# Kernel optimization log

Measured on AMD Instinct MI355X. Metric: run time of the kernel, lower is better.

The kernel has to match this reference:

```python
import jax, jax.numpy as jnp
import numpy as np

VOCAB = 128000
SEED = 42
BATCH = 256
SEQ = 128
BIAS_FACTOR = 2.0
TOP_P = 0.9


def setup_inputs() -> dict:
    key = jax.random.key(0)
    k1, k2 = jax.random.split(key)
    input_ids = jax.random.randint(k1, (BATCH, SEQ), 0, VOCAB, dtype=jnp.int64 if jax.config.jax_enable_x64 else jnp.int32)
    scores = jax.random.normal(k2, (BATCH, VOCAB), dtype=jnp.float32) * 4.0
    # green list generated exactly as in the torch module: numpy rng, 0/1 per vocab entry
    green = jnp.asarray(np.random.default_rng(SEED).integers(0, 2, VOCAB), dtype=jnp.float32)
    return {"input_ids": input_ids, "scores": scores, "green": green}


def reference(input_ids, scores, green):
    B, V = scores.shape
    # bias green tokens, softmax over vocab
    logits = scores + BIAS_FACTOR * green[None, :]          # [B, V]
    probs = jax.nn.softmax(logits, axis=-1)                 # [B, V]
    # descending sort (torch.sort(descending=True))
    sorted_idx = jnp.argsort(-probs, axis=-1)               # [B, V]
    sorted_probs = jnp.take_along_axis(probs, sorted_idx, axis=-1)
    cum = jnp.cumsum(sorted_probs, axis=-1)                 # [B, V]
    # torch.searchsorted(cum, top_p, right=False): first i with cum[i] >= top_p
    cutoff = jnp.sum(cum < TOP_P, axis=-1, keepdims=True)   # [B, 1]
    # keep positions 0..cutoff inclusive (original zeroes cutoff+1:)
    keep = jnp.arange(V)[None, :] <= cutoff                 # [B, V]
    kept = jnp.where(keep, sorted_probs, 0.0)
    kept = kept / jnp.sum(kept, axis=-1, keepdims=True)
    kept = jnp.where(jnp.isfinite(kept), kept, 0.0)
    # multinomial(1) over truncated renormalized probs
    samp = jax.random.categorical(jax.random.key(1), jnp.log(kept), axis=-1)  # [B]
    next_tok = jnp.take_along_axis(sorted_idx, samp[:, None], axis=-1)[:, 0]  # [B]
    # scores[b,:] = 1e-5; scores[b, next_token] = 1e5
    out = jnp.full((B, V), 1e-5, dtype=scores.dtype)
    out = out.at[jnp.arange(B), next_tok].set(1e5)
    return out
```

## Files before the change

### kernel.cpp

```cpp
#include <hip/hip_runtime.h>
#include <cstdint>
#include <cstddef>

#define BATCH 256
#define VOCAB 128000
#define V4 (VOCAB/4)
#define NBINS 4096
#define CAP 4096
#define WSEG 256
#define NSEG 32
#define SPILLCAP 6144
#define GATE_SPILL 8.0f
#define SPILL_BIN 3088u
#define GATE_HIST 1.0f
#define M44 0xFFFFFFFFFFFull
#define FIX 16777216.0f
#define FIXINV 5.9604644775390625e-8f

__device__ __forceinline__ uint32_t rotl32(uint32_t v, int r){ return (v<<r)|(v>>(32-r)); }

__device__ __forceinline__ void threefry2x32_01(uint32_t& x0, uint32_t& x1){
  const uint32_t ks0=0u, ks1=1u, ks2=0x1BD11BDAu ^ 0u ^ 1u;
  x0+=ks0; x1+=ks1;
#define TF_R(r) { x0+=x1; x1=rotl32(x1,(r)); x1^=x0; }
  TF_R(13) TF_R(15) TF_R(26) TF_R(6)
  x0+=ks1; x1+=ks2+1u;
  TF_R(17) TF_R(29) TF_R(16) TF_R(24)
  x0+=ks2; x1+=ks0+2u;
  TF_R(13) TF_R(15) TF_R(26) TF_R(6)
  x0+=ks0; x1+=ks1+3u;
  TF_R(17) TF_R(29) TF_R(16) TF_R(24)
  x0+=ks1; x1+=ks2+4u;
  TF_R(13) TF_R(15) TF_R(26) TF_R(6)
  x0+=ks2; x1+=ks0+5u;
#undef TF_R
}

__device__ __forceinline__ float gumbel_at(uint32_t z){
  uint32_t x0 = 0u, x1 = z;
  threefry2x32_01(x0, x1);
  uint32_t bits = x0 ^ x1;
  uint32_t fb = (bits >> 9) | 0x3F800000u;
  float f = __uint_as_float(fb) - 1.0f;
  const float tiny = 1.17549435e-38f;
  float uu = fmaxf(tiny, f + tiny);
  return -logf(-logf(uu));
}

__device__ __forceinline__ uint32_t fkey(uint32_t u){
  return (u >> 31) ? ~u : (u | 0x80000000u);
}
__device__ __forceinline__ float pdecode(unsigned long long k){
  return __uint_as_float(~(uint32_t)(k >> 32));
}

__global__ __launch_bounds__(256) void k_stream(
    const float* __restrict__ scores, const float* __restrict__ green,
    float* __restrict__ out, unsigned long long* __restrict__ spill,
    unsigned* __restrict__ counts, float* __restrict__ pmax,
    float* __restrict__ psum)
{
  const int blk = blockIdx.x;
  const int b = blk >> 3, q = blk & 7;
  const int tid = threadIdx.x, lane = tid & 63, wv = tid >> 6;
  const int base = q * 4000;
  const float4* row4 = (const float4*)(scores + (size_t)b * VOCAB);
  const float4* grn4 = (const float4*)green;
  float4* o4 = (float4*)(out + (size_t)b * VOCAB);
  const int sidx = (q << 2) | wv;
  unsigned long long* seg = spill + ((size_t)b * NSEG + sidx) * WSEG;
  const float4 fv = make_float4(1e-5f, 1e-5f, 1e-5f, 1e-5f);

  float lm = -INFINITY, ls16 = 0.f;
  unsigned wcnt = 0u;

#define SP1(LV, IDX) do { \
    float l_ = (LV); \
    lm = fmaxf(lm, l_); \
    ls16 += expf(l_ - 16.0f); \
    bool pr_ = (l_ >= GATE_SPILL); \
    unsigned long long mk_ = __ballot(pr_); \
    if (pr_){ \
      unsigned pos_ = wcnt + (unsigned)__popcll(mk_ & ((1ull << lane) - 1ull)); \
      if (pos_ < WSEG) \
        seg[pos_] = ((unsigned long long)__float_as_uint(l_) << 32) | (IDX); \
    } \
    wcnt += (unsigned)__popcll(mk_); \
  } while(0)

#define SP4(SV, GV, II) do { \
    SP1(fmaf(2.f, (GV).x, (SV).x), (unsigned)(4*(II)+0)); \
    SP1(fmaf(2.f, (GV).y, (SV).y), (unsigned)(4*(II)+1)); \
    SP1(fmaf(2.f, (GV).z, (SV).z), (unsigned)(4*(II)+2)); \
    SP1(fmaf(2.f, (GV).w, (SV).w), (unsigned)(4*(II)+3)); \
  } while(0)

  for (int g = 0; g < 3; ++g){
    const int i0 = base + tid + g*1024, i1 = i0+256, i2 = i0+512, i3 = i0+768;
    float4 sa = row4[i0], sb = row4[i1], sc = row4[i2], sd = row4[i3];
    float4 ga = grn4[i0], gb = grn4[i1], gc = grn4[i2], gd = grn4[i3];
    o4[i0] = fv; o4[i1] = fv; o4[i2] = fv; o4[i3] = fv;
    SP4(sa, ga, i0); SP4(sb, gb, i1); SP4(sc, gc, i2); SP4(sd, gd, i3);
  }
  {
    const int i0 = base + 3072 + tid, i1 = i0+256, i2 = i0+512;
    float4 sa = row4[i0], sb = row4[i1], sc = row4[i2];
    float4 ga = grn4[i0], gb = grn4[i1], gc = grn4[i2];
    o4[i0] = fv; o4[i1] = fv; o4[i2] = fv;
    SP4(sa, ga, i0); SP4(sb, gb, i1); SP4(sc, gc, i2);
  }
  if (tid < 160){
    const int i0 = base + 3840 + tid;
    float4 sa = row4[i0];
    float4 ga = grn4[i0];
    o4[i0] = fv;
    SP4(sa, ga, i0);
  }
#undef SP4
#undef SP1

  for (int off = 32; off > 0; off >>= 1){
    lm = fmaxf(lm, __shfl_down(lm, off, 64));
    ls16 += __shfl_down(ls16, off, 64);
  }
  if (lane == 0){
    const int gi = b * NSEG + sidx;
    pmax[gi] = lm; psum[gi] = ls16; counts[gi] = wcnt;
  }
}

__global__ __launch_bounds__(1024) void k_row(
    const float* __restrict__ scores, const float* __restrict__ green,
    float* __restrict__ out, const unsigned long long* __restrict__ spill,
    const unsigned* __restrict__ counts, const float* __restrict__ pmax,
    const float* __restrict__ psum)
{
  __shared__ unsigned long long sp64[SPILLCAP];
  __shared__ union {
    unsigned long long hist[NBINS];
    unsigned long long skeys[CAP];
  } u;
  __shared__ float red[1024];
  __shared__ unsigned long long wavewin[16];
  __shared__ unsigned segoff[NSEG + 1];
  __shared__ float m_sh, s16_sh;
  __shared__ unsigned n_sh, thr_sh, fb_sh;
  __shared__ int cut_sh;

  const int b = blockIdx.x, tid = threadIdx.x;
  const float* srow = scores + (size_t)b * VOCAB;
  float* orow = out + (size_t)b * VOCAB;

  for (int i = tid; i < NBINS; i += 1024) u.hist[i] = 0ull;
  if (tid == 0){
    unsigned tot = 0u, fb = 0u;
    float mm = -INFINITY, ss = 0.f;
    for (int s = 0; s < NSEG; ++s){
      unsigned c = counts[b*NSEG + s];
      segoff[s] = tot;
      if (c > WSEG) fb = 1u;
      tot += c;
      mm = fmaxf(mm, pmax[b*NSEG + s]);
      ss += psum[b*NSEG + s];
    }
    segoff[NSEG] = tot;
    if (tot > SPILLCAP) fb = 1u;
    m_sh = mm; s16_sh = ss; fb_sh = fb; n_sh = 0u;
  }
  __syncthreads();
  const float m = m_sh, S16 = s16_sh;
  const unsigned tot = segoff[NSEG];
  unsigned fb = fb_sh;

  if (!fb){
    for (int s = 0; s < NSEG; ++s){
      const unsigned c0 = segoff[s], cl = segoff[s+1] - c0;
      const unsigned long long* seg = spill + ((size_t)b*NSEG + s)*WSEG;
      for (unsigned j = tid; j < cl; j += 1024) sp64[c0 + j] = seg[j];
    }
    __syncthreads();
    for (unsigned j = tid; j < tot; j += 1024){
      uint32_t lb = (uint32_t)(sp64[j] >> 32);
      atomicAdd(&u.hist[fkey(lb) >> 20],
                (1ull<<44) | (unsigned long long)(expf(__uint_as_float(lb) - 16.0f) * FIX));
    }
    __syncthreads();
    if (tid == 0){
      float target = 0.903f * S16;
      int top = (int)(fkey(__float_as_uint(m)) >> 20);
      float acc = 0.f; unsigned c = 0; unsigned result = (unsigned)top;
      for (int bin = top; bin >= 0; --bin){
        unsigned long long h = u.hist[bin];
        unsigned cb = (unsigned)(h >> 44);
        if (c + cb > CAP) break;
        acc += (float)(h & M44) * FIXINV; c += cb; result = (unsigned)bin;
        if (acc >= target){
          if (bin > 0 && c + (unsigned)(u.hist[bin-1] >> 44) <= CAP)
            result = (unsigned)(bin-1);
          break;
        }
      }
      thr_sh = result;
      if (result < SPILL_BIN) fb_sh = 1u;
    }
    __syncthreads();
    fb = fb_sh;
  }

  if (fb){
    for (int i = tid; i < NBINS; i += 1024) u.hist[i] = 0ull;
    __syncthreads();
    const float4* row4 = (const float4*)srow;
    const float4* grn4 = (const float4*)green;
    for (int i = tid; i < V4; i += 1024){
      float4 s = row4[i], g = grn4[i];
      #pragma unroll
      for (int c = 0; c < 4; ++c){
        float l = fmaf(2.f, (&g.x)[c], (&s.x)[c]);
        if (l >= GATE_HIST)
          atomicAdd(&u.hist[fkey(__float_as_uint(l)) >> 20],
                    (1ull<<44) | (unsigned long long)(expf(l - 16.0f) * FIX));
      }
    }
    __syncthreads();
    if (tid == 0){
      float target = 0.903f * S16;
      int top = (int)(fkey(__float_as_uint(m)) >> 20);
      float acc = 0.f; unsigned c = 0; unsigned result = (unsigned)top;
      for (int bin = top; bin >= 0; --bin){
        unsigned long long h = u.hist[bin];
        unsigned cb = (unsigned)(h >> 44);
        if (c + cb > CAP) break;
        acc += (float)(h & M44) * FIXINV; c += cb; result = (unsigned)bin;
        if (acc >= target){
          if (bin > 0 && c + (unsigned)(u.hist[bin-1] >> 44) <= CAP)
            result = (unsigned)(bin-1);
          break;
        }
      }
      thr_sh = result;
    }
    __syncthreads();
    const unsigned thr = thr_sh;
    for (int i = tid; i < V4; i += 1024){
      float4 s = row4[i], g = grn4[i];
      #pragma unroll
      for (int c = 0; c < 4; ++c){
        float l = fmaf(2.f, (&g.x)[c], (&s.x)[c]);
        if ((fkey(__float_as_uint(l)) >> 20) >= thr){
          unsigned pos = atomicAdd(&n_sh, 1u);
          float p = expf(l - 16.0f) / S16;
          if (pos < CAP)
            u.skeys[pos] = ((unsigned long long)(~__float_as_uint(p)) << 32) | (unsigned)(4*i + c);
        }
      }
    }
  } else {
    const unsigned thr = thr_sh;
    for (unsigned j = tid; j < tot; j += 1024){
      unsigned long long k = sp64[j];
      uint32_t lb = (uint32_t)(k >> 32);
      if ((fkey(lb) >> 20) >= thr){
        unsigned pos = atomicAdd(&n_sh, 1u);
        float p = expf(__uint_as_float(lb) - 16.0f) / S16;
        if (pos < CAP)
          u.skeys[pos] = ((unsigned long long)(~__float_as_uint(p)) << 32) | (k & 0xFFFFFFFFull);
      }
    }
  }
  __syncthreads();
  unsigned n = n_sh; if (n > CAP) n = CAP;

  unsigned N2 = 2; while (N2 < n) N2 <<= 1;
  for (unsigned i = n + tid; i < N2; i += 1024) u.skeys[i] = 0xFFFFFFFFFFFFFFFFull;
  __syncthreads();
  for (unsigned k = 2; k <= N2; k <<= 1){
    for (unsigned j = k >> 1; j > 0; j >>= 1){
      for (unsigned i = tid; i < N2; i += 1024){
        unsigned ixj = i ^ j;
        if (ixj > i){
          unsigned long long a = u.skeys[i], c2 = u.skeys[ixj];
          bool up = ((i & k) == 0u);
          if ((a > c2) == up){ u.skeys[i] = c2; u.skeys[ixj] = a; }
        }
      }
      __syncthreads();
    }
  }

  unsigned C = (n + 1023) >> 10;
  {
    unsigned lo = tid * C; if (lo > n) lo = n;
    unsigned hi = lo + C;  if (hi > n) hi = n;
    float s = 0.f;
    for (unsigned j = lo; j < hi; ++j) s += pdecode(u.skeys[j]);
    red[tid] = s;
  }
  __syncthreads();
  if (tid == 0){
    float run = 0.f; int cut = (int)n - 1; int t = 0;
    for (; t < 1024; ++t){ float cs = red[t]; if (run + cs >= 0.9f) break; run += cs; }
    if (t < 1024){
      float c2 = run;
      for (unsigned j = (unsigned)t * C; j < n; ++j){
        c2 += pdecode(u.skeys[j]);
        if (c2 >= 0.9f){ cut = (int)j; break; }
      }
    }
    cut_sh = cut;
  }
  __syncthreads();
  const int cut = cut_sh;

  float best = -INFINITY; unsigned bj = 0x7FFFFFFFu;
  for (int j = tid; j <= cut; j += 1024){
    float p = pdecode(u.skeys[j]);
    float sc = logf(p) + gumbel_at((uint32_t)b * (uint32_t)VOCAB + (uint32_t)j);
    if (sc > best || (sc == best && (unsigned)j < bj)){ best = sc; bj = (unsigned)j; }
  }
  for (int off = 32; off > 0; off >>= 1){
    float osc = __shfl_down(best, off, 64);
    unsigned oj = __shfl_down(bj, off, 64);
    if (osc > best || (osc == best && oj < bj)){ best = osc; bj = oj; }
  }
  if ((tid & 63) == 0){
    uint32_t ub = __float_as_uint(best);
    uint32_t ou = (ub >> 31) ? ~ub : (ub | 0x80000000u);
    wavewin[tid >> 6] = ((unsigned long long)ou << 32) |
                        (unsigned long long)(0xFFFFFFFFu - bj);
  }
  __syncthreads();
  if (tid == 0){
    unsigned long long bb = 0ull;
    for (int w = 0; w < 16; ++w){ unsigned long long x = wavewin[w]; if (x > bb) bb = x; }
    unsigned jwin = 0xFFFFFFFFu - (unsigned)(bb & 0xFFFFFFFFull);
    orow[(size_t)(u.skeys[jwin] & 0xFFFFFFFFull)] = 1e5f;
  }
}

extern "C" void kernel_launch(void* const* d_in, const int* in_sizes, int n_in,
                              void* d_out, int out_size, void* d_ws, size_t ws_size,
                              hipStream_t stream) {
  const float* scores = (const float*)d_in[1];
  const float* green  = (const float*)d_in[2];
  float* out = (float*)d_out;

  unsigned long long* spill = (unsigned long long*)d_ws;
  unsigned* counts = (unsigned*)(spill + (size_t)BATCH * NSEG * WSEG);
  float* pmax = (float*)(counts + BATCH * NSEG);
  float* psum = pmax + BATCH * NSEG;
  (void)ws_size;

  hipLaunchKernelGGL(k_stream, dim3(BATCH*8), dim3(256),  0, stream,
                     scores, green, out, spill, counts, pmax, psum);
  hipLaunchKernelGGL(k_row,    dim3(BATCH),   dim3(1024), 0, stream,
                     scores, green, out, spill, counts, pmax, psum);
}
```

Measured before the change: 342.3 us.

## Software-pipeline stream loads, add occupancy hint, drop extra threshold bin

The streaming kernel now issues the next group's score and green loads before processing the current group, a register double-buffer meant to hide global memory latency. A launch-bounds occupancy hint of 4 blocks per CU is added. The threshold search in the row kernel no longer widens the candidate set by one extra histogram bin, which shrinks the candidate set to sort. That bin was a safety margin against approximate histogram sums, so dropping it risks correctness near the top-p cutoff, and the extra live registers could reduce occupancy.

```diff
diff --git a/kernel.cpp b/kernel.cpp
--- a/kernel.cpp
+++ b/kernel.cpp
@@ -54,7 +54,7 @@
   return __uint_as_float(~(uint32_t)(k >> 32));
 }
 
-__global__ __launch_bounds__(256) void k_stream(
+__global__ __launch_bounds__(256, 4) void k_stream(
     const float* __restrict__ scores, const float* __restrict__ green,
     float* __restrict__ out, unsigned long long* __restrict__ spill,
     unsigned* __restrict__ counts, float* __restrict__ pmax,
@@ -95,26 +95,40 @@
     SP1(fmaf(2.f, (GV).w, (SV).w), (unsigned)(4*(II)+3)); \
   } while(0)
 
+  float4 sa, sb, sc, sd, ga, gb, gc, gd;
+  {
+    const int i0 = base + tid;
+    sa = row4[i0]; sb = row4[i0+256]; sc = row4[i0+512]; sd = row4[i0+768];
+    ga = grn4[i0]; gb = grn4[i0+256]; gc = grn4[i0+512]; gd = grn4[i0+768];
+  }
+  #pragma unroll
   for (int g = 0; g < 3; ++g){
-    const int i0 = base + tid + g*1024, i1 = i0+256, i2 = i0+512, i3 = i0+768;
-    float4 sa = row4[i0], sb = row4[i1], sc = row4[i2], sd = row4[i3];
-    float4 ga = grn4[i0], gb = grn4[i1], gc = grn4[i2], gd = grn4[i3];
-    o4[i0] = fv; o4[i1] = fv; o4[i2] = fv; o4[i3] = fv;
-    SP4(sa, ga, i0); SP4(sb, gb, i1); SP4(sc, gc, i2); SP4(sd, gd, i3);
+    const int cur = base + tid + g*1024;
+    const int nxt = cur + 1024;
+    float4 ta, tb, tc, td, ua, ub, uc, ud;
+    if (g < 2){
+      ta = row4[nxt]; tb = row4[nxt+256]; tc = row4[nxt+512]; td = row4[nxt+768];
+      ua = grn4[nxt]; ub = grn4[nxt+256]; uc = grn4[nxt+512]; ud = grn4[nxt+768];
+    } else {
+      ta = row4[nxt]; tb = row4[nxt+256]; tc = row4[nxt+512];
+      ua = grn4[nxt]; ub = grn4[nxt+256]; uc = grn4[nxt+512];
+      td = tc; ud = uc;
+    }
+    o4[cur] = fv; o4[cur+256] = fv; o4[cur+512] = fv; o4[cur+768] = fv;
+    SP4(sa, ga, cur); SP4(sb, gb, cur+256); SP4(sc, gc, cur+512); SP4(sd, gd, cur+768);
+    sa = ta; sb = tb; sc = tc; sd = td; ga = ua; gb = ub; gc = uc; gd = ud;
   }
   {
-    const int i0 = base + 3072 + tid, i1 = i0+256, i2 = i0+512;
-    float4 sa = row4[i0], sb = row4[i1], sc = row4[i2];
-    float4 ga = grn4[i0], gb = grn4[i1], gc = grn4[i2];
-    o4[i0] = fv; o4[i1] = fv; o4[i2] = fv;
-    SP4(sa, ga, i0); SP4(sb, gb, i1); SP4(sc, gc, i2);
+    const int i0 = base + 3072 + tid;
+    o4[i0] = fv; o4[i0+256] = fv; o4[i0+512] = fv;
+    SP4(sa, ga, i0); SP4(sb, gb, i0+256); SP4(sc, gc, i0+512);
   }
   if (tid < 160){
     const int i0 = base + 3840 + tid;
-    float4 sa = row4[i0];
-    float4 ga = grn4[i0];
+    float4 s = row4[i0];
+    float4 g = grn4[i0];
     o4[i0] = fv;
-    SP4(sa, ga, i0);
+    SP4(s, g, i0);
   }
 #undef SP4
 #undef SP1
@@ -194,11 +208,7 @@
         unsigned cb = (unsigned)(h >> 44);
         if (c + cb > CAP) break;
         acc += (float)(h & M44) * FIXINV; c += cb; result = (unsigned)bin;
-        if (acc >= target){
-          if (bin > 0 && c + (unsigned)(u.hist[bin-1] >> 44) <= CAP)
-            result = (unsigned)(bin-1);
-          break;
-        }
+        if (acc >= target) break;
       }
       thr_sh = result;
       if (result < SPILL_BIN) fb_sh = 1u;
@@ -232,11 +242,7 @@
         unsigned cb = (unsigned)(h >> 44);
         if (c + cb > CAP) break;
         acc += (float)(h & M44) * FIXINV; c += cb; result = (unsigned)bin;
-        if (acc >= target){
-          if (bin > 0 && c + (unsigned)(u.hist[bin-1] >> 44) <= CAP)
-            result = (unsigned)(bin-1);
-          break;
-        }
+        if (acc >= target) break;
       }
       thr_sh = result;
     }
```

Measured after the change: 332.4 us. -2.9%, faster.
